# Kernel tuning notes

Hardware: AMD Instinct MI355X
Metric: run time of the kernel (lower is better)

## Reference

```python
import jax, jax.numpy as jnp
import numpy as np


def setup_inputs() -> dict:
    key = jax.random.key(0)
    k1, k2, k3 = jax.random.split(key, 3)
    B, T, Din, D = 32, 2048, 256, 256
    x = jax.random.normal(k1, (B, T, Din), dtype=jnp.float32)
    # glorot-ish scaling for stability
    W = jax.random.normal(k2, (Din, 4 * D), dtype=jnp.float32) * (1.0 / np.sqrt(Din))
    U = jax.random.normal(k3, (D, 4 * D), dtype=jnp.float32) * (1.0 / np.sqrt(D))
    b = jnp.zeros((4 * D,), dtype=jnp.float32)
    return {"x": x, "W": W, "U": U, "b": b}


def reference(x, W, U, b):
    # x: [B, T, Din]; W: [Din, 4D]; U: [D, 4D]; b: [4D]
    # Gate slice order (per original step()): 0=i, 1=f, 2=o, 3=candidate
    D = U.shape[0]
    B = x.shape[0]
    # Precompute input projections for all timesteps in one big matmul.
    px = jnp.einsum('btd,df->tbf', x, W) + b  # [T, B, 4D]

    def step(carry, px_t):
        h, c = carry
        preact = px_t + h @ U  # [B, 4D]
        i = jax.nn.sigmoid(preact[:, 0 * D:1 * D])
        f = jax.nn.sigmoid(preact[:, 1 * D:2 * D])
        o = jax.nn.sigmoid(preact[:, 2 * D:3 * D])
        g = jnp.tanh(preact[:, 3 * D:4 * D])
        c_new = f * c + i * g
        h_new = o * jnp.tanh(c_new)
        return (h_new, c_new), h_new

    h0 = jnp.zeros((B, D), dtype=x.dtype)
    c0 = jnp.zeros((B, D), dtype=x.dtype)
    _, h_seq = jax.lax.scan(step, (h0, c0), px)  # h_seq: [T, B, D]
    return jnp.transpose(h_seq, (1, 0, 2))  # output_sequence: [B, T, D]
```

## Files before the change

### kernel.cpp

```cpp
#include <hip/hip_runtime.h>
#include <math.h>

#define B_SZ 32
#define T_SZ 2048
#define DIN 256
#define DH 256
#define FOUR_D 1024

#define NW 8
#define DPW 32

#define IK16(k) ((k) + ((k) >> 6) * 8)
#define USTR 264

typedef _Float16 f16x2 __attribute__((ext_vector_type(2)));

#if __has_builtin(__builtin_amdgcn_fdot2)
#define FDOT2(a, b, c) __builtin_amdgcn_fdot2((a), (b), (c), false)
#else
__device__ __forceinline__ float fdot2_emu(f16x2 a, f16x2 b, float c) {
    return c + (float)a[0] * (float)b[0] + (float)a[1] * (float)b[1];
}
#define FDOT2(a, b, c) fdot2_emu((a), (b), (c))
#endif

__device__ __forceinline__ f16x2 H2(float f) {
    union { float f; f16x2 h; } u; u.f = f; return u.h;
}

__global__ void zero_ws(unsigned int* p, int n) {
    int i = blockIdx.x * blockDim.x + threadIdx.x;
    if (i < n) p[i] = 0u;
}

__global__ __launch_bounds__(512, 2) void lstm_fused4(
    const float* __restrict__ x, const float* __restrict__ W,
    const float* __restrict__ U, const float* __restrict__ bias,
    float* __restrict__ out, unsigned long long* __restrict__ hbuf)
{
    __shared__ _Float16 u_lds[128 * USTR];
    __shared__ _Float16 w_lds[128 * USTR];
    __shared__ _Float16 h1_lds[2][288];
    __shared__ _Float16 x_lds[2][288];

    const int b = blockIdx.x >> 3;
    const int w = blockIdx.x & 7;
    const int tid = threadIdx.x;
    const int dd = tid >> 4;
    const int gate = (tid >> 2) & 3;
    const int seg = tid & 3;
    const int colg = (gate << 8) + (w << 5) + dd;
    const int d = (w << 5) + dd;
    const bool pub = (tid & 15) == 0;

    for (int it = 0; it < 64; ++it) {
        int lin = (it << 9) + tid;
        int row = lin & 127;
        int kk = lin >> 7;
        int gcol = ((row & 3) << 8) + (w << 5) + (row >> 2);
        int sg = kk >> 6;
        int cc = (kk >> 3) & 7;
        int jj = kk & 7;
        int p = ((cc >> 1) << 3) + (sg << 1) + (cc & 1);
        int idx = row * USTR + (p << 3) + jj;
        u_lds[idx] = (_Float16)U[(size_t)kk * FOUR_D + gcol];
        w_lds[idx] = (_Float16)W[(size_t)kk * FOUR_D + gcol];
    }
    float4 xr = make_float4(0.f, 0.f, 0.f, 0.f);
    if (tid < 64) {
        float4 v0 = *(const float4*)&x[((size_t)b * T_SZ) * DIN + tid * 4];
        _Float16* dst = &x_lds[0][IK16(tid * 4)];
        dst[0] = (_Float16)v0.x; dst[1] = (_Float16)v0.y;
        dst[2] = (_Float16)v0.z; dst[3] = (_Float16)v0.w;
        xr = *(const float4*)&x[((size_t)b * T_SZ + 1) * DIN + tid * 4];
    }
    const float binit = (seg == 0) ? bias[colg] : 0.0f;
    float c_reg = 0.0f;
    __syncthreads();

    const int rowb = (dd * 4 + gate) * USTR;
    float4 uq[8];
#pragma unroll
    for (int c2 = 0; c2 < 8; ++c2) {
        int p = ((c2 >> 1) << 3) + (seg << 1) + (c2 & 1);
        uq[c2] = *(const float4*)&u_lds[rowb + (p << 3)];
    }
#pragma unroll
    for (int c2 = 0; c2 < 8; ++c2) {
        asm volatile("" : "+v"(uq[c2].x), "+v"(uq[c2].y),
                          "+v"(uq[c2].z), "+v"(uq[c2].w));
    }

    for (int tt = 0; tt < T_SZ; ++tt) {
        if (tid < 64) {
            if (tt + 1 < T_SZ) {
                _Float16* dst = &x_lds[(tt + 1) & 1][IK16(tid * 4)];
                dst[0] = (_Float16)xr.x; dst[1] = (_Float16)xr.y;
                dst[2] = (_Float16)xr.z; dst[3] = (_Float16)xr.w;
            }
            if (tt + 2 < T_SZ)
                xr = *(const float4*)&x[((size_t)b * T_SZ + tt + 2) * DIN + tid * 4];
        }

        const _Float16* xrow = &x_lds[tt & 1][seg * 72];
        float a0 = binit, a1 = 0.f, a2 = 0.f, a3 = 0.f;
#pragma unroll
        for (int c2 = 0; c2 < 8; ++c2) {
            int p = ((c2 >> 1) << 3) + (seg << 1) + (c2 & 1);
            float4 wv = *(const float4*)&w_lds[rowb + (p << 3)];
            float4 xv = *(const float4*)&xrow[c2 << 3];
            a0 = FDOT2(H2(wv.x), H2(xv.x), a0);
            a1 = FDOT2(H2(wv.y), H2(xv.y), a1);
            a2 = FDOT2(H2(wv.z), H2(xv.z), a2);
            a3 = FDOT2(H2(wv.w), H2(xv.w), a3);
        }

        if (tid < DH) {
            const bool local = (tid >> 5) == w;
            if (tt == 0) {
                h1_lds[0][IK16(tid)] = (_Float16)0.0f;
            } else if (!local) {
                const unsigned long long want = (unsigned long long)(unsigned)tt;
                const unsigned long long* slot = hbuf +
                    (((size_t)(tt & 1) * B_SZ + b) * DH + tid);
                unsigned long long v;
                do {
                    v = __hip_atomic_load(slot, __ATOMIC_RELAXED,
                                          __HIP_MEMORY_SCOPE_AGENT);
                } while ((v >> 32) != want);
                h1_lds[tt & 1][IK16(tid)] = (_Float16)__uint_as_float((unsigned)v);
            }
        }
        __syncthreads();

        const _Float16* hrow = &h1_lds[tt & 1][seg * 72];
#pragma unroll
        for (int c2 = 0; c2 < 8; ++c2) {
            float4 hv = *(const float4*)&hrow[c2 << 3];
            a0 = FDOT2(H2(uq[c2].x), H2(hv.x), a0);
            a1 = FDOT2(H2(uq[c2].y), H2(hv.y), a1);
            a2 = FDOT2(H2(uq[c2].z), H2(hv.z), a2);
            a3 = FDOT2(H2(uq[c2].w), H2(hv.w), a3);
        }
        float pr = (a0 + a1) + (a2 + a3);

        pr += __shfl_xor(pr, 1);
        pr += __shfl_xor(pr, 2);
        float pre = pr;

        float act;
        if (gate < 3) {
            act = 1.0f / (1.0f + __expf(-pre));
        } else {
            float e = __expf(-2.0f * pre);
            act = 2.0f / (1.0f + e) - 1.0f;
        }

        const int bl = (tid & 48) | seg;
        float ig = __shfl(act, bl);
        float fg = __shfl(act, bl | 4);
        float og = __shfl(act, bl | 8);
        float gv = __shfl(act, bl | 12);

        float cn = fg * c_reg + ig * gv;
        c_reg = cn;
        float ec = __expf(-2.0f * cn);
        float hn = og * (2.0f / (1.0f + ec) - 1.0f);

        if (pub) {
            unsigned long long pv =
                ((unsigned long long)(unsigned)(tt + 1) << 32) |
                (unsigned long long)__float_as_uint(hn);
            __hip_atomic_store(hbuf + (((size_t)((tt + 1) & 1) * B_SZ + b) * DH + d),
                               pv, __ATOMIC_RELAXED, __HIP_MEMORY_SCOPE_AGENT);
            h1_lds[(tt + 1) & 1][IK16(d)] = (_Float16)hn;
            out[((size_t)b * T_SZ + tt) * DH + d] = hn;
        }
    }
}

extern "C" void kernel_launch(void* const* d_in, const int* in_sizes, int n_in,
                              void* d_out, int out_size, void* d_ws, size_t ws_size,
                              hipStream_t stream) {
    const float* x    = (const float*)d_in[0];
    const float* W    = (const float*)d_in[1];
    const float* U    = (const float*)d_in[2];
    const float* bias = (const float*)d_in[3];
    float* out = (float*)d_out;

    unsigned long long* hbuf = (unsigned long long*)d_ws;

    int zero_words = (128 * 1024) / 4;
    zero_ws<<<(zero_words + 255) / 256, 256, 0, stream>>>((unsigned int*)d_ws, zero_words);

    lstm_fused4<<<B_SZ * NW, 512, 0, stream>>>(x, W, U, bias, out, hbuf);
}
```

Before: 2.988 ms.

## Offload input projection to back-half threads so front threads poll h immediately

Threads 256-511 now compute the W·x input projection for their own gate column and for a partner column, with W held in registers instead of re-read from LDS. They hand the partner result to threads 0-255 through a shared wacc buffer. The front threads only poll the cross-block hidden-state buffer, so the projection work is taken off their path before the barrier. This adds 64 more live VGPRs per back thread, which risks spills under the 512x2 launch bounds, and it puts extra FDOT2 work and an LDS exchange on the back half.

```diff
diff --git a/kernel.cpp b/kernel.cpp
--- a/kernel.cpp
+++ b/kernel.cpp
@@ -8,7 +8,6 @@
 #define FOUR_D 1024
 
 #define NW 8
-#define DPW 32
 
 #define IK16(k) ((k) + ((k) >> 6) * 8)
 #define USTR 264
@@ -33,7 +32,7 @@
     if (i < n) p[i] = 0u;
 }
 
-__global__ __launch_bounds__(512, 2) void lstm_fused4(
+__global__ __launch_bounds__(512, 2) void lstm_fused6(
     const float* __restrict__ x, const float* __restrict__ W,
     const float* __restrict__ U, const float* __restrict__ bias,
     float* __restrict__ out, unsigned long long* __restrict__ hbuf)
@@ -42,6 +41,7 @@
     __shared__ _Float16 w_lds[128 * USTR];
     __shared__ _Float16 h1_lds[2][288];
     __shared__ _Float16 x_lds[2][288];
+    __shared__ float    wacc[2][256];
 
     const int b = blockIdx.x >> 3;
     const int w = blockIdx.x & 7;
@@ -52,6 +52,10 @@
     const int colg = (gate << 8) + (w << 5) + dd;
     const int d = (w << 5) + dd;
     const bool pub = (tid & 15) == 0;
+    const bool back = (tid >= 256);
+
+    const int dd_par = (dd - 16) & 31;
+    const int colg_par = (gate << 8) + (w << 5) + dd_par;
 
     for (int it = 0; it < 64; ++it) {
         int lin = (it << 9) + tid;
@@ -67,19 +71,21 @@
         w_lds[idx] = (_Float16)W[(size_t)kk * FOUR_D + gcol];
     }
     float4 xr = make_float4(0.f, 0.f, 0.f, 0.f);
-    if (tid < 64) {
-        float4 v0 = *(const float4*)&x[((size_t)b * T_SZ) * DIN + tid * 4];
-        _Float16* dst = &x_lds[0][IK16(tid * 4)];
+    if (tid >= 448) {
+        int l = tid - 448;
+        float4 v0 = *(const float4*)&x[((size_t)b * T_SZ) * DIN + l * 4];
+        _Float16* dst = &x_lds[0][IK16(l * 4)];
         dst[0] = (_Float16)v0.x; dst[1] = (_Float16)v0.y;
         dst[2] = (_Float16)v0.z; dst[3] = (_Float16)v0.w;
-        xr = *(const float4*)&x[((size_t)b * T_SZ + 1) * DIN + tid * 4];
-    }
-    const float binit = (seg == 0) ? bias[colg] : 0.0f;
+        xr = *(const float4*)&x[((size_t)b * T_SZ + 1) * DIN + l * 4];
+    }
+    const float binit_own = (seg == 0) ? bias[colg] : 0.0f;
+    const float binit_par = (seg == 0) ? bias[colg_par] : 0.0f;
     float c_reg = 0.0f;
     __syncthreads();
 
     const int rowb = (dd * 4 + gate) * USTR;
-    float4 uq[8];
+    float4 uq[8], wqo[8], wqp[8];
 #pragma unroll
     for (int c2 = 0; c2 < 8; ++c2) {
         int p = ((c2 >> 1) << 3) + (seg << 1) + (c2 & 1);
@@ -90,32 +96,55 @@
         asm volatile("" : "+v"(uq[c2].x), "+v"(uq[c2].y),
                           "+v"(uq[c2].z), "+v"(uq[c2].w));
     }
-
-    for (int tt = 0; tt < T_SZ; ++tt) {
-        if (tid < 64) {
-            if (tt + 1 < T_SZ) {
-                _Float16* dst = &x_lds[(tt + 1) & 1][IK16(tid * 4)];
-                dst[0] = (_Float16)xr.x; dst[1] = (_Float16)xr.y;
-                dst[2] = (_Float16)xr.z; dst[3] = (_Float16)xr.w;
-            }
-            if (tt + 2 < T_SZ)
-                xr = *(const float4*)&x[((size_t)b * T_SZ + tt + 2) * DIN + tid * 4];
-        }
-
-        const _Float16* xrow = &x_lds[tt & 1][seg * 72];
-        float a0 = binit, a1 = 0.f, a2 = 0.f, a3 = 0.f;
+    if (back) {
+        const int rowb_par = (dd_par * 4 + gate) * USTR;
 #pragma unroll
         for (int c2 = 0; c2 < 8; ++c2) {
             int p = ((c2 >> 1) << 3) + (seg << 1) + (c2 & 1);
-            float4 wv = *(const float4*)&w_lds[rowb + (p << 3)];
-            float4 xv = *(const float4*)&xrow[c2 << 3];
-            a0 = FDOT2(H2(wv.x), H2(xv.x), a0);
-            a1 = FDOT2(H2(wv.y), H2(xv.y), a1);
-            a2 = FDOT2(H2(wv.z), H2(xv.z), a2);
-            a3 = FDOT2(H2(wv.w), H2(xv.w), a3);
-        }
-
-        if (tid < DH) {
+            wqo[c2] = *(const float4*)&w_lds[rowb + (p << 3)];
+            wqp[c2] = *(const float4*)&w_lds[rowb_par + (p << 3)];
+        }
+#pragma unroll
+        for (int c2 = 0; c2 < 8; ++c2) {
+            asm volatile("" : "+v"(wqo[c2].x), "+v"(wqo[c2].y),
+                              "+v"(wqo[c2].z), "+v"(wqo[c2].w));
+            asm volatile("" : "+v"(wqp[c2].x), "+v"(wqp[c2].y),
+                              "+v"(wqp[c2].z), "+v"(wqp[c2].w));
+        }
+    }
+
+    for (int tt = 0; tt < T_SZ; ++tt) {
+        float wown = 0.0f;
+
+        if (back) {
+            if (tid >= 448) {
+                int l = tid - 448;
+                if (tt + 1 < T_SZ) {
+                    _Float16* dst = &x_lds[(tt + 1) & 1][IK16(l * 4)];
+                    dst[0] = (_Float16)xr.x; dst[1] = (_Float16)xr.y;
+                    dst[2] = (_Float16)xr.z; dst[3] = (_Float16)xr.w;
+                }
+                if (tt + 2 < T_SZ)
+                    xr = *(const float4*)&x[((size_t)b * T_SZ + tt + 2) * DIN + l * 4];
+            }
+            const _Float16* xrow = &x_lds[tt & 1][seg * 72];
+            float a0 = binit_own, a1 = 0.f, a2 = 0.f, a3 = 0.f;
+            float b0 = binit_par, b1 = 0.f, b2 = 0.f, b3 = 0.f;
+#pragma unroll
+            for (int c2 = 0; c2 < 8; ++c2) {
+                float4 xv = *(const float4*)&xrow[c2 << 3];
+                a0 = FDOT2(H2(wqo[c2].x), H2(xv.x), a0);
+                a1 = FDOT2(H2(wqo[c2].y), H2(xv.y), a1);
+                a2 = FDOT2(H2(wqo[c2].z), H2(xv.z), a2);
+                a3 = FDOT2(H2(wqo[c2].w), H2(xv.w), a3);
+                b0 = FDOT2(H2(wqp[c2].x), H2(xv.x), b0);
+                b1 = FDOT2(H2(wqp[c2].y), H2(xv.y), b1);
+                b2 = FDOT2(H2(wqp[c2].z), H2(xv.z), b2);
+                b3 = FDOT2(H2(wqp[c2].w), H2(xv.w), b3);
+            }
+            wown = (a0 + a1) + (a2 + a3);
+            wacc[tt & 1][tid - 256] = (b0 + b1) + (b2 + b3);
+        } else {
             const bool local = (tid >> 5) == w;
             if (tt == 0) {
                 h1_lds[0][IK16(tid)] = (_Float16)0.0f;
@@ -134,6 +163,8 @@
         __syncthreads();
 
         const _Float16* hrow = &h1_lds[tt & 1][seg * 72];
+        float a0 = back ? wown : wacc[tt & 1][tid];
+        float a1 = 0.f, a2 = 0.f, a3 = 0.f;
 #pragma unroll
         for (int c2 = 0; c2 < 8; ++c2) {
             float4 hv = *(const float4*)&hrow[c2 << 3];
@@ -193,5 +224,5 @@
     int zero_words = (128 * 1024) / 4;
     zero_ws<<<(zero_words + 255) / 256, 256, 0, stream>>>((unsigned int*)d_ws, zero_words);
 
-    lstm_fused4<<<B_SZ * NW, 512, 0, stream>>>(x, W, U, bias, out, hbuf);
-}
+    lstm_fused6<<<B_SZ * NW, 512, 0, stream>>>(x, W, U, bias, out, hbuf);
+}
```

New measurement: 3.111 ms. +4.1%, slower.
